# Optimization experiments

Hardware: AMD Instinct MI355X
Metric: run time of the kernel (lower is better)

The kernel has to match this reference:

```python
import jax, jax.numpy as jnp
import numpy as np

N = 400000      # total atoms across batch of molecules
E = 1600000     # directed edges (avg degree 4)
G = 4096        # number of graphs (molecules)
F_IN = 78       # atomic feature size
H = 128         # gnn hidden dims (gnn_0 = gnn_1 = 128)
FF0, FF1 = 256, 128


def _lin(k, fan_in, fan_out):
    return jax.random.normal(k, (fan_in, fan_out), jnp.float32) / np.sqrt(fan_in).astype(np.float32)


def setup_inputs() -> dict:
    key = jax.random.key(0)
    ks = jax.random.split(key, 10)
    x = jax.random.normal(ks[0], (N, F_IN), jnp.float32)
    edge_index = jax.random.randint(ks[1], (2, E), 0, N, dtype=jnp.int64)
    # sorted graph ids, guaranteed non-empty segments (empty segment -> -inf under max pool)
    batch = (jnp.arange(N, dtype=jnp.int64) * G) // N
    return {
        'x': x, 'edge_index': edge_index, 'batch': batch,
        'W0': _lin(ks[2], F_IN, H), 'b0': jnp.zeros((H,), jnp.float32),
        'W1': _lin(ks[3], H, H),    'b1': jnp.zeros((H,), jnp.float32),
        'Wf0': _lin(ks[4], H, FF0), 'bf0': jnp.zeros((FF0,), jnp.float32),
        'Wf1': _lin(ks[5], FF0, FF1), 'bf1': jnp.zeros((FF1,), jnp.float32),
    }


def _gcn_conv(h, W, b, src, dst, dinv):
    # GCNConv with add_self_loops=True, symmetric normalization.
    hw = h @ W                                     # [N, out]
    norm = dinv[src] * dinv[dst]                   # [E]
    msg = hw[src] * norm[:, None]                  # gather + scale
    agg = jax.ops.segment_sum(msg, dst, num_segments=h.shape[0])
    agg = agg + hw * (dinv * dinv)[:, None]        # self-loop contribution
    return agg + b


def reference(x, edge_index, batch, W0, b0, W1, b1, Wf0, bf0, Wf1, bf1):
    src, dst = edge_index[0], edge_index[1]
    # degree of A + I computed at target nodes (PyG gcn_norm uses col)
    deg = jax.ops.segment_sum(jnp.ones((E,), x.dtype), dst, num_segments=N) + 1.0
    dinv = jax.lax.rsqrt(deg)

    h = jax.nn.relu(_gcn_conv(x, W0, b0, src, dst, dinv))
    h = jax.nn.relu(_gcn_conv(h, W1, b1, src, dst, dinv))

    g = jax.ops.segment_max(h, batch, num_segments=G)   # global max pool [G, H]

    g = jax.nn.relu(g @ Wf0 + bf0)   # dropout is identity in eval
    g = jax.nn.relu(g @ Wf1 + bf1)
    return g
```

## Files before the change

kernel.cpp:

```cpp
#include <hip/hip_runtime.h>
#include <cstdint>
#include <cstddef>

#define NATOMS 400000
#define NEDGES 1600000
#define NGRAPH 4096
#define F_INN  78
#define HDIM   128
#define FF0D   256
#define FF1D   128

#define XPAD   80

typedef __attribute__((ext_vector_type(8))) short short8;
typedef __attribute__((ext_vector_type(4))) short short4v;
typedef __attribute__((ext_vector_type(4))) float f32x4;
typedef __attribute__((ext_vector_type(2))) float f32x2;

static __device__ __forceinline__ short f2bf(float f) {
    unsigned u = __builtin_bit_cast(unsigned, f);
    unsigned r = (u + 0x7fffu + ((u >> 16) & 1u)) >> 16;
    return (short)r;
}
static __device__ __forceinline__ float bf2f(unsigned short u) {
    return __builtin_bit_cast(float, ((unsigned)u) << 16);
}

__global__ __launch_bounds__(256) void k_degi(const int* __restrict__ dst,
                                              int* __restrict__ deg,
                                              int* __restrict__ rank, int E) {
    int e = blockIdx.x * 256 + threadIdx.x;
    if (e < E) rank[e] = atomicAdd(&deg[dst[e]], 1);
}

__global__ __launch_bounds__(256) void k_scan1(int* __restrict__ data,
                                               int* __restrict__ blockSums,
                                               float* __restrict__ dinv, int n) {
    __shared__ int ts[256];
    const int base = blockIdx.x * 1024 + threadIdx.x * 4;
    int v[4];
    #pragma unroll
    for (int j = 0; j < 4; ++j) v[j] = (base + j < n) ? data[base + j] : 0;
    #pragma unroll
    for (int j = 0; j < 4; ++j)
        if (base + j < n) dinv[base + j] = rsqrtf((float)v[j] + 1.0f);
    const int tot = v[0] + v[1] + v[2] + v[3];
    ts[threadIdx.x] = tot;
    __syncthreads();
    #pragma unroll
    for (int off = 1; off < 256; off <<= 1) {
        int t = (threadIdx.x >= off) ? ts[threadIdx.x - off] : 0;
        __syncthreads();
        ts[threadIdx.x] += t;
        __syncthreads();
    }
    int run = ts[threadIdx.x] - tot;
    #pragma unroll
    for (int j = 0; j < 4; ++j) {
        if (base + j < n) data[base + j] = run;
        run += v[j];
    }
    if (threadIdx.x == 255) blockSums[blockIdx.x] = ts[255];
}

__global__ __launch_bounds__(512) void k_scan2(int* __restrict__ blockSums, int nb) {
    __shared__ int ts[512];
    int v = (threadIdx.x < nb) ? blockSums[threadIdx.x] : 0;
    ts[threadIdx.x] = v;
    __syncthreads();
    #pragma unroll
    for (int off = 1; off < 512; off <<= 1) {
        int t = (threadIdx.x >= off) ? ts[threadIdx.x - off] : 0;
        __syncthreads();
        ts[threadIdx.x] += t;
        __syncthreads();
    }
    if (threadIdx.x < nb) blockSums[threadIdx.x] = ts[threadIdx.x] - v;
}

__global__ __launch_bounds__(256) void k_scan3(int* __restrict__ data,
                                               const int* __restrict__ blockSums,
                                               int n, int total) {
    const int off = blockSums[blockIdx.x];
    const int base = blockIdx.x * 1024 + threadIdx.x * 4;
    #pragma unroll
    for (int j = 0; j < 4; ++j)
        if (base + j < n) data[base + j] += off;
    if (blockIdx.x == 0 && threadIdx.x == 0) data[n] = total;
}

__global__ __launch_bounds__(256) void k_fill(const int* __restrict__ src,
                                              const int* __restrict__ dst,
                                              const int* __restrict__ row_start,
                                              const int* __restrict__ rank,
                                              int2* __restrict__ csr_ev,
                                              const float* __restrict__ dinv, int E) {
    int e = blockIdx.x * 256 + threadIdx.x;
    if (e >= E) return;
    int d = dst[e];
    int s = src[e];
    int pos = row_start[d] + rank[e];
    float norm = dinv[s] * dinv[d];
    csr_ev[pos] = make_int2(s, __builtin_bit_cast(int, norm));
}

template<int KC, int KSRC, bool BIASROW>
__global__ __launch_bounds__(64) void k_packw(const float* __restrict__ W,
                                              const float* __restrict__ b,
                                              short* __restrict__ wf) {
    int t = blockIdx.x * 64 + threadIdx.x;
    int f = t >> 6, lane = t & 63;
    int ct = f / KC, kc = f % KC;
    int n  = ct * 16 + (lane & 15);
    int k0 = kc * 32 + (lane >> 4) * 8;
    short8 o;
    #pragma unroll
    for (int j = 0; j < 8; ++j) {
        int k = k0 + j;
        float v = 0.f;
        if (k < KSRC) v = W[(size_t)k * 128 + n];
        else if (BIASROW && k == KSRC) v = b[n];
        o[j] = f2bf(v);
    }
    *(short8*)(wf + (size_t)t * 8) = o;
}

__global__ __launch_bounds__(256) void k_packx(const float* __restrict__ x,
                                               unsigned short* __restrict__ xb) {
    int t = blockIdx.x * 256 + threadIdx.x;
    if (t >= NATOMS * 20) return;
    int n = t / 20, g = t % 20;
    const float* xr = x + (size_t)n * F_INN + g * 4;
    short4v o;
    if (g < 19) {
        f32x2 a = *(const f32x2*)(xr);
        f32x2 b = *(const f32x2*)(xr + 2);
        o.x = f2bf(a.x); o.y = f2bf(a.y); o.z = f2bf(b.x); o.w = f2bf(b.y);
    } else {
        f32x2 a = *(const f32x2*)(xr);
        o.x = f2bf(a.x); o.y = f2bf(a.y); o.z = 0; o.w = 0;
    }
    *(short4v*)(xb + (size_t)n * XPAD + g * 4) = o;
}

__global__ __launch_bounds__(256) void k_fused0(
    const unsigned short* __restrict__ xb, const short* __restrict__ wfrag,
    const int* __restrict__ row_start, const int2* __restrict__ csr_ev,
    const float* __restrict__ dinv, short* __restrict__ outp)
{
    constexpr int XLDS = 104;
    __shared__ short lds_w[24 * 64 * 8];
    __shared__ __align__(16) unsigned short xs[32 * XLDS];
    __shared__ __align__(16) char lds_st[4 * 2048];

    const int tid = threadIdx.x;
    #pragma unroll
    for (int it = 0; it < 6; ++it) {
        int t = it * 256 + tid;
        *(short8*)(lds_w + (size_t)t * 8) = *(const short8*)(wfrag + (size_t)t * 8);
    }

    {
        const int nl = tid >> 3;
        const int n  = blockIdx.x * 32 + nl;
        const int l  = tid & 7;
        const int c8 = l * 8;
        const int ct = 64 + l * 2;
        const float dv = dinv[n];
        const float d2 = dv * dv;

        float acc[8], tacc0, tacc1;
        {
            const short8 sv = *(const short8*)(xb + (size_t)n * XPAD + c8);
            const unsigned tv = *(const unsigned*)(xb + (size_t)n * XPAD + ct);
            #pragma unroll
            for (int j = 0; j < 8; ++j) acc[j] = bf2f((unsigned short)sv[j]) * d2;
            tacc0 = bf2f((unsigned short)(tv & 0xffff)) * d2;
            tacc1 = bf2f((unsigned short)(tv >> 16)) * d2;
        }

        const int s0 = row_start[n], s1 = row_start[n + 1];
        int i = s0;
        for (; i + 3 < s1; i += 4) {
            const int2 e0 = csr_ev[i];
            const int2 e1 = csr_ev[i + 1];
            const int2 e2 = csr_ev[i + 2];
            const int2 e3 = csr_ev[i + 3];
            const short8 r0 = *(const short8*)(xb + (size_t)e0.x * XPAD + c8);
            const short8 r1 = *(const short8*)(xb + (size_t)e1.x * XPAD + c8);
            const short8 r2 = *(const short8*)(xb + (size_t)e2.x * XPAD + c8);
            const short8 r3 = *(const short8*)(xb + (size_t)e3.x * XPAD + c8);
            const unsigned t0 = *(const unsigned*)(xb + (size_t)e0.x * XPAD + ct);
            const unsigned t1 = *(const unsigned*)(xb + (size_t)e1.x * XPAD + ct);
            const unsigned t2 = *(const unsigned*)(xb + (size_t)e2.x * XPAD + ct);
            const unsigned t3 = *(const unsigned*)(xb + (size_t)e3.x * XPAD + ct);
            const float w0 = __builtin_bit_cast(float, e0.y);
            const float w1 = __builtin_bit_cast(float, e1.y);
            const float w2 = __builtin_bit_cast(float, e2.y);
            const float w3 = __builtin_bit_cast(float, e3.y);
            #pragma unroll
            for (int j = 0; j < 8; ++j) acc[j] = fmaf(bf2f((unsigned short)r0[j]), w0, acc[j]);
            #pragma unroll
            for (int j = 0; j < 8; ++j) acc[j] = fmaf(bf2f((unsigned short)r1[j]), w1, acc[j]);
            #pragma unroll
            for (int j = 0; j < 8; ++j) acc[j] = fmaf(bf2f((unsigned short)r2[j]), w2, acc[j]);
            #pragma unroll
            for (int j = 0; j < 8; ++j) acc[j] = fmaf(bf2f((unsigned short)r3[j]), w3, acc[j]);
            tacc0 = fmaf(bf2f((unsigned short)(t0 & 0xffff)), w0, tacc0);
            tacc1 = fmaf(bf2f((unsigned short)(t0 >> 16)),    w0, tacc1);
            tacc0 = fmaf(bf2f((unsigned short)(t1 & 0xffff)), w1, tacc0);
            tacc1 = fmaf(bf2f((unsigned short)(t1 >> 16)),    w1, tacc1);
            tacc0 = fmaf(bf2f((unsigned short)(t2 & 0xffff)), w2, tacc0);
            tacc1 = fmaf(bf2f((unsigned short)(t2 >> 16)),    w2, tacc1);
            tacc0 = fmaf(bf2f((unsigned short)(t3 & 0xffff)), w3, tacc0);
            tacc1 = fmaf(bf2f((unsigned short)(t3 >> 16)),    w3, tacc1);
        }
        for (; i < s1; ++i) {
            const int2 e0 = csr_ev[i];
            const short8 r0 = *(const short8*)(xb + (size_t)e0.x * XPAD + c8);
            const unsigned t0 = *(const unsigned*)(xb + (size_t)e0.x * XPAD + ct);
            const float w0 = __builtin_bit_cast(float, e0.y);
            #pragma unroll
            for (int j = 0; j < 8; ++j) acc[j] = fmaf(bf2f((unsigned short)r0[j]), w0, acc[j]);
            tacc0 = fmaf(bf2f((unsigned short)(t0 & 0xffff)), w0, tacc0);
            tacc1 = fmaf(bf2f((unsigned short)(t0 >> 16)),    w0, tacc1);
        }

        short8 o;
        #pragma unroll
        for (int j = 0; j < 8; ++j) o[j] = f2bf(acc[j]);
        *(short8*)(xs + nl * XLDS + c8) = o;
        unsigned to;
        if (l == 7) to = 0x00003F80u;
        else {
            to = (unsigned)(unsigned short)f2bf(tacc0) |
                 ((unsigned)(unsigned short)f2bf(tacc1) << 16);
        }
        *(unsigned*)(xs + nl * XLDS + ct) = to;
        *(unsigned*)(xs + nl * XLDS + 80 + l * 2) = 0u;
    }
    __syncthreads();

    const int lane = tid & 63;
    const int wid  = tid >> 6;
    const int m = lane & 15, q = lane >> 4;
    const int T  = wid >> 1;
    const int c0 = (wid & 1) * 4;

    short8 afr[3];
    #pragma unroll
    for (int kc = 0; kc < 3; ++kc)
        afr[kc] = *(const short8*)(xs + (T * 16 + m) * XLDS + kc * 32 + q * 8);

    f32x4 acc[4];
    #pragma unroll
    for (int cc = 0; cc < 4; ++cc) acc[cc] = (f32x4){0.f, 0.f, 0.f, 0.f};
    #pragma unroll
    for (int kc = 0; kc < 3; ++kc)
        #pragma unroll
        for (int cc = 0; cc < 4; ++cc) {
            const short8 wv = *(const short8*)(lds_w + ((size_t)(((c0 + cc) * 3 + kc) * 64 + lane)) * 8);
            acc[cc] = __builtin_amdgcn_mfma_f32_16x16x32_bf16(wv, afr[kc], acc[cc], 0, 0, 0);
        }

    char* const st = lds_st + wid * 2048;
    #pragma unroll
    for (int cc = 0; cc < 4; ++cc) {
        short4v o;
        o.x = f2bf(fmaxf(acc[cc][0], 0.f));
        o.y = f2bf(fmaxf(acc[cc][1], 0.f));
        o.z = f2bf(fmaxf(acc[cc][2], 0.f));
        o.w = f2bf(fmaxf(acc[cc][3], 0.f));
        const int c = (cc * 32 + q * 8) ^ ((m & 7) << 4);
        *(short4v*)(st + m * 128 + c) = o;
    }
    #pragma unroll
    for (int p = 0; p < 2; ++p) {
        const int r  = p * 8 + (lane >> 3);
        const int cb = ((lane & 7) * 16) ^ ((r & 7) << 4);
        const short8 v = *(const short8*)(st + r * 128 + cb);
        *(short8*)(outp + (size_t)(blockIdx.x * 32 + T * 16 + r) * 128
                        + c0 * 16 + (lane & 7) * 8) = v;
    }
}

template<int KC, int KSRC, bool RELU>
__global__ __launch_bounds__(256) void k_gemm_mfma(
    const short* __restrict__ inv, const short* __restrict__ wfrag,
    short* __restrict__ outp, int M)
{
    constexpr int NFRAG = 8 * KC;
    __shared__ short lds_w[NFRAG * 64 * 8];
    __shared__ __align__(16) char lds_st[4 * 4096];

    const int tid = threadIdx.x;
    #pragma unroll
    for (int it = 0; it < NFRAG * 64 / 256; ++it) {
        int t = it * 256 + tid;
        *(short8*)(lds_w + (size_t)t * 8) = *(const short8*)(wfrag + (size_t)t * 8);
    }
    __syncthreads();

    const int lane = tid & 63;
    const int m = lane & 15, q = lane >> 4;
    const int wid = tid >> 6;
    const int gw = blockIdx.x * 4 + wid;
    const int NW = gridDim.x * 4;
    const int NTILE = M / 16;
    char* const st = lds_st + wid * 4096;

    auto tile_mma = [&](int t, const short8* afr) {
        f32x4 acc[8];
        #pragma unroll
        for (int ct = 0; ct < 8; ++ct) acc[ct] = (f32x4){0.f, 0.f, 0.f, 0.f};
        #pragma unroll
        for (int kc = 0; kc < KC; ++kc)
            #pragma unroll
            for (int ct = 0; ct < 8; ++ct) {
                const short8 wv = *(const short8*)(lds_w + ((size_t)((ct * KC + kc) * 64 + lane)) * 8);
                acc[ct] = __builtin_amdgcn_mfma_f32_16x16x32_bf16(wv, afr[kc], acc[ct], 0, 0, 0);
            }
        #pragma unroll
        for (int ct = 0; ct < 8; ++ct) {
            short4v o;
            float v0 = acc[ct][0], v1 = acc[ct][1], v2 = acc[ct][2], v3 = acc[ct][3];
            if constexpr (RELU) {
                v0 = fmaxf(v0, 0.f); v1 = fmaxf(v1, 0.f);
                v2 = fmaxf(v2, 0.f); v3 = fmaxf(v3, 0.f);
            }
            o.x = f2bf(v0); o.y = f2bf(v1); o.z = f2bf(v2); o.w = f2bf(v3);
            const int c = (ct * 32 + q * 8) ^ ((m & 7) << 4);
            *(short4v*)(st + m * 256 + c) = o;
        }
        #pragma unroll
        for (int p = 0; p < 4; ++p) {
            const int r = p * 4 + (lane >> 4);
            const int c = ((lane & 15) * 16) ^ ((r & 7) << 4);
            const short8 v = *(const short8*)(st + r * 256 + c);
            *(short8*)(outp + (size_t)(t * 16 + r) * 128 + (lane & 15) * 8) = v;
        }
    };

    short8 fA[KC], fB[KC];
    auto load_to = [&](int tile, short8* b) {
        const short* xr = inv + (size_t)(tile * 16 + m) * KSRC;
        #pragma unroll
        for (int kc = 0; kc < KC; ++kc) {
            const int k0 = kc * 32 + q * 8;
            short8 v = {0, 0, 0, 0, 0, 0, 0, 0};
            if (k0 + 8 <= KSRC) v = *(const short8*)(xr + k0);
            b[kc] = v;
        }
    };

    load_to(gw, fA);
    for (int t = gw; t < NTILE; t += NW) {
        const int tn = t + NW;
        if (tn < NTILE) load_to(tn, fB);
        tile_mma(t, fA);
        #pragma unroll
        for (int kc = 0; kc < KC; ++kc) fA[kc] = fB[kc];
    }
}

__global__ __launch_bounds__(256) void k_gather_pool(
    const unsigned short* __restrict__ hw,
    const int* __restrict__ row_start, const int2* __restrict__ csr_ev,
    const float* __restrict__ dinv, const float* __restrict__ bias,
    const int* __restrict__ batch, int* __restrict__ pool, int half)
{
    const int n  = blockIdx.x * 32 + (threadIdx.x >> 3);
    const int c8 = half * 64 + (threadIdx.x & 7) * 8;
    const float dv = dinv[n];
    const float d2 = dv * dv;

    float acc[8];
    {
        const short8 sv = *(const short8*)(hw + (size_t)n * HDIM + c8);
        #pragma unroll
        for (int j = 0; j < 8; ++j)
            acc[j] = fmaf(bf2f((unsigned short)sv[j]), d2, bias[c8 + j]);
    }

    const int s0 = row_start[n], s1 = row_start[n + 1];
    int i = s0;
    for (; i + 3 < s1; i += 4) {
        const int2 e0 = csr_ev[i];
        const int2 e1 = csr_ev[i + 1];
        const int2 e2 = csr_ev[i + 2];
        const int2 e3 = csr_ev[i + 3];
        const short8 r0 = *(const short8*)(hw + (size_t)e0.x * HDIM + c8);
        const short8 r1 = *(const short8*)(hw + (size_t)e1.x * HDIM + c8);
        const short8 r2 = *(const short8*)(hw + (size_t)e2.x * HDIM + c8);
        const short8 r3 = *(const short8*)(hw + (size_t)e3.x * HDIM + c8);
        const float w0 = __builtin_bit_cast(float, e0.y);
        const float w1 = __builtin_bit_cast(float, e1.y);
        const float w2 = __builtin_bit_cast(float, e2.y);
        const float w3 = __builtin_bit_cast(float, e3.y);
        #pragma unroll
        for (int j = 0; j < 8; ++j) acc[j] = fmaf(bf2f((unsigned short)r0[j]), w0, acc[j]);
        #pragma unroll
        for (int j = 0; j < 8; ++j) acc[j] = fmaf(bf2f((unsigned short)r1[j]), w1, acc[j]);
        #pragma unroll
        for (int j = 0; j < 8; ++j) acc[j] = fmaf(bf2f((unsigned short)r2[j]), w2, acc[j]);
        #pragma unroll
        for (int j = 0; j < 8; ++j) acc[j] = fmaf(bf2f((unsigned short)r3[j]), w3, acc[j]);
    }
    for (; i < s1; ++i) {
        const int2 e0 = csr_ev[i];
        const short8 r0 = *(const short8*)(hw + (size_t)e0.x * HDIM + c8);
        const float w0 = __builtin_bit_cast(float, e0.y);
        #pragma unroll
        for (int j = 0; j < 8; ++j) acc[j] = fmaf(bf2f((unsigned short)r0[j]), w0, acc[j]);
    }

    const int gbase = batch[blockIdx.x * 32];
    const int glast = batch[blockIdx.x * 32 + 31];
    const int idx   = batch[n] - gbase;

    float red[2][8];
    #pragma unroll
    for (int s = 0; s < 2; ++s)
        #pragma unroll
        for (int j = 0; j < 8; ++j)
            red[s][j] = (idx == s) ? fmaxf(acc[j], 0.f) : 0.f;

    #pragma unroll
    for (int msk = 8; msk <= 32; msk <<= 1)
        #pragma unroll
        for (int s = 0; s < 2; ++s)
            #pragma unroll
            for (int j = 0; j < 8; ++j)
                red[s][j] = fmaxf(red[s][j], __shfl_xor(red[s][j], msk));

    __shared__ float sm[4][2][64];
    const int wid  = threadIdx.x >> 6;
    const int lane = threadIdx.x & 63;
    if (lane < 8) {
        #pragma unroll
        for (int s = 0; s < 2; ++s)
            #pragma unroll
            for (int j = 0; j < 8; ++j)
                sm[wid][s][lane * 8 + j] = red[s][j];
    }
    __syncthreads();
    if (threadIdx.x < 128) {
        const int s = threadIdx.x >> 6;
        const int f = threadIdx.x & 63;
        if (s == 0 || glast != gbase) {
            float m = fmaxf(fmaxf(sm[0][s][f], sm[1][s][f]),
                            fmaxf(sm[2][s][f], sm[3][s][f]));
            atomicMax(pool + (size_t)(gbase + s) * HDIM + half * 64 + f,
                      __builtin_bit_cast(int, m));
        }
    }
}

template<int K, int NC, bool OUT_RELU_BIAS>
__global__ __launch_bounds__(256) void k_gemm(
    const float* __restrict__ in, const float* __restrict__ W,
    const float* __restrict__ out_bias, float* __restrict__ out0, int M)
{
    constexpr int BK = 32;
    constexpr int TC = NC / 8;
    constexpr int TR = 256 / TC;
    constexpr int ROWS = TR * 8;
    constexpr int XST = ROWS + 4;

    __shared__ float xs[BK][XST];
    __shared__ float ws[BK][NC];

    const int tid = threadIdx.x;
    const int tc  = tid % TC;
    const int tr  = tid / TC;
    const int row0 = blockIdx.x * ROWS;

    float acc[8][8];
    #pragma unroll
    for (int i = 0; i < 8; ++i)
        #pragma unroll
        for (int j = 0; j < 8; ++j) acc[i][j] = 0.f;

    for (int k0 = 0; k0 < K; k0 += BK) {
        {
            constexpr int TASKS = BK * NC / 4;
            #pragma unroll
            for (int it = 0; it < TASKS / 256; ++it) {
                int t  = it * 256 + tid;
                int wk = t / (NC / 4);
                int wc = (t % (NC / 4)) * 4;
                *(float4*)(&ws[wk][wc]) = *(const float4*)(W + (size_t)(k0 + wk) * NC + wc);
            }
        }
        {
            constexpr int TASKS = ROWS * BK / 4;
            #pragma unroll
            for (int it = 0; it < TASKS / 256; ++it) {
                int t   = it * 256 + tid;
                int r   = t / (BK / 4);
                int kq  = (t % (BK / 4)) * 4;
                float4 x4 = *(const float4*)(in + (size_t)(row0 + r) * K + k0 + kq);
                xs[kq + 0][r] = x4.x; xs[kq + 1][r] = x4.y;
                xs[kq + 2][r] = x4.z; xs[kq + 3][r] = x4.w;
            }
        }
        __syncthreads();
        #pragma unroll 8
        for (int kk = 0; kk < BK; ++kk) {
            float a[8], b[8];
            #pragma unroll
            for (int i = 0; i < 8; ++i) a[i] = xs[kk][tr * 8 + i];
            #pragma unroll
            for (int j = 0; j < 8; ++j) b[j] = ws[kk][tc * 8 + j];
            #pragma unroll
            for (int i = 0; i < 8; ++i)
                #pragma unroll
                for (int j = 0; j < 8; ++j)
                    acc[i][j] = fmaf(a[i], b[j], acc[i][j]);
        }
        __syncthreads();
    }

    #pragma unroll
    for (int i = 0; i < 8; ++i) {
        const int row = row0 + tr * 8 + i;
        #pragma unroll
        for (int jq = 0; jq < 2; ++jq) {
            const int col = tc * 8 + jq * 4;
            float4 v;
            v.x = acc[i][jq * 4 + 0]; v.y = acc[i][jq * 4 + 1];
            v.z = acc[i][jq * 4 + 2]; v.w = acc[i][jq * 4 + 3];
            if constexpr (OUT_RELU_BIAS) {
                const float4 bb = *(const float4*)(out_bias + col);
                v.x = fmaxf(v.x + bb.x, 0.f); v.y = fmaxf(v.y + bb.y, 0.f);
                v.z = fmaxf(v.z + bb.z, 0.f); v.w = fmaxf(v.w + bb.w, 0.f);
            }
            *(float4*)(out0 + (size_t)row * NC + col) = v;
        }
    }
}

extern "C" void kernel_launch(void* const* d_in, const int* in_sizes, int n_in,
                              void* d_out, int out_size, void* d_ws, size_t ws_size,
                              hipStream_t stream) {
    const float* x    = (const float*)d_in[0];
    const int*   ei   = (const int*)d_in[1];
    const int*   batch= (const int*)d_in[2];
    const float* W0   = (const float*)d_in[3];
    const float* b0   = (const float*)d_in[4];
    const float* W1   = (const float*)d_in[5];
    const float* b1   = (const float*)d_in[6];
    const float* Wf0  = (const float*)d_in[7];
    const float* bf0  = (const float*)d_in[8];
    const float* Wf1  = (const float*)d_in[9];
    const float* bf1  = (const float*)d_in[10];
    float* out = (float*)d_out;

    const int* srcI = ei;
    const int* dstI = ei + NEDGES;

    constexpr int SCAN_NBLK = (NATOMS + 1023) / 1024;

    char* base = (char*)d_ws;
    unsigned short* hwA  = (unsigned short*)(base + 0);
    int*   rank      = (int*)(base + 0);
    unsigned short* aggB = (unsigned short*)(base + 102400000);
    float* dinv      = (float*)(base + 204800000);
    int*   row_start = (int*)(base + 206400000);
    int2*  csr_ev    = (int2*)(base + 208000064);
    int*   blockSums = (int*)(base + 220800064);
    float* pool      = (float*)(base + 220802112);
    float* ff0       = (float*)(base + 222899264);
    short* wf0       = (short*)(base + 227093568);
    short* wf1       = (short*)(base + 227118144);
    unsigned short* xb = (unsigned short*)(base + 227150912);

    hipMemsetAsync(row_start, 0, (size_t)(NATOMS + 1) * sizeof(int), stream);
    hipMemsetAsync(pool, 0, (size_t)NGRAPH * HDIM * sizeof(float), stream);
    k_degi<<<(NEDGES + 255) / 256, 256, 0, stream>>>(dstI, row_start, rank, NEDGES);
    k_scan1<<<SCAN_NBLK, 256, 0, stream>>>(row_start, blockSums, dinv, NATOMS);
    k_scan2<<<1, 512, 0, stream>>>(blockSums, SCAN_NBLK);
    k_scan3<<<SCAN_NBLK, 256, 0, stream>>>(row_start, blockSums, NATOMS, NEDGES);
    k_fill<<<(NEDGES + 255) / 256, 256, 0, stream>>>(srcI, dstI, row_start, rank,
                                                     csr_ev, dinv, NEDGES);

    k_packw<3, F_INN, true><<<8 * 3, 64, 0, stream>>>(W0, b0, wf0);
    k_packw<4, HDIM, false><<<8 * 4, 64, 0, stream>>>(W1, nullptr, wf1);
    k_packx<<<(NATOMS * 20 + 255) / 256, 256, 0, stream>>>(x, xb);

    k_fused0<<<NATOMS / 32, 256, 0, stream>>>(xb, wf0, row_start, csr_ev, dinv,
                                              (short*)aggB);

    k_gemm_mfma<4, HDIM, false><<<1024, 256, 0, stream>>>((const short*)aggB, wf1,
                                                          (short*)hwA, NATOMS);
    k_gather_pool<<<NATOMS / 32, 256, 0, stream>>>(hwA, row_start, csr_ev,
                                                   dinv, b1, batch, (int*)pool, 0);
    k_gather_pool<<<NATOMS / 32, 256, 0, stream>>>(hwA, row_start, csr_ev,
                                                   dinv, b1, batch, (int*)pool, 1);

    k_gemm<HDIM, FF0D, true><<<NGRAPH / 64, 256, 0, stream>>>(pool, Wf0, bf0, ff0, NGRAPH);
    k_gemm<FF0D, FF1D, true><<<NGRAPH / 128, 256, 0, stream>>>(ff0, Wf1, bf1, out, NGRAPH);
}
```

Measured before the change: 658.1 us.

## Fuse layer-2 aggregation, W1 GEMM and max-pool into one kernel

```diff
diff --git a/kernel.cpp b/kernel.cpp
--- a/kernel.cpp
+++ b/kernel.cpp
@@ -149,7 +149,7 @@
     const float* __restrict__ dinv, short* __restrict__ outp)
 {
     constexpr int XLDS = 104;
-    __shared__ short lds_w[24 * 64 * 8];
+    __shared__ __align__(16) short lds_w[24 * 64 * 8];
     __shared__ __align__(16) unsigned short xs[32 * XLDS];
     __shared__ __align__(16) char lds_st[4 * 2048];
 
@@ -284,174 +284,155 @@
     }
 }
 
-template<int KC, int KSRC, bool RELU>
-__global__ __launch_bounds__(256) void k_gemm_mfma(
-    const short* __restrict__ inv, const short* __restrict__ wfrag,
-    short* __restrict__ outp, int M)
-{
-    constexpr int NFRAG = 8 * KC;
-    __shared__ short lds_w[NFRAG * 64 * 8];
-    __shared__ __align__(16) char lds_st[4 * 4096];
-
-    const int tid = threadIdx.x;
-    #pragma unroll
-    for (int it = 0; it < NFRAG * 64 / 256; ++it) {
-        int t = it * 256 + tid;
-        *(short8*)(lds_w + (size_t)t * 8) = *(const short8*)(wfrag + (size_t)t * 8);
-    }
-    __syncthreads();
-
-    const int lane = tid & 63;
-    const int m = lane & 15, q = lane >> 4;
-    const int wid = tid >> 6;
-    const int gw = blockIdx.x * 4 + wid;
-    const int NW = gridDim.x * 4;
-    const int NTILE = M / 16;
-    char* const st = lds_st + wid * 4096;
-
-    auto tile_mma = [&](int t, const short8* afr) {
-        f32x4 acc[8];
-        #pragma unroll
-        for (int ct = 0; ct < 8; ++ct) acc[ct] = (f32x4){0.f, 0.f, 0.f, 0.f};
-        #pragma unroll
-        for (int kc = 0; kc < KC; ++kc)
-            #pragma unroll
-            for (int ct = 0; ct < 8; ++ct) {
-                const short8 wv = *(const short8*)(lds_w + ((size_t)((ct * KC + kc) * 64 + lane)) * 8);
-                acc[ct] = __builtin_amdgcn_mfma_f32_16x16x32_bf16(wv, afr[kc], acc[ct], 0, 0, 0);
-            }
-        #pragma unroll
-        for (int ct = 0; ct < 8; ++ct) {
-            short4v o;
-            float v0 = acc[ct][0], v1 = acc[ct][1], v2 = acc[ct][2], v3 = acc[ct][3];
-            if constexpr (RELU) {
-                v0 = fmaxf(v0, 0.f); v1 = fmaxf(v1, 0.f);
-                v2 = fmaxf(v2, 0.f); v3 = fmaxf(v3, 0.f);
-            }
-            o.x = f2bf(v0); o.y = f2bf(v1); o.z = f2bf(v2); o.w = f2bf(v3);
-            const int c = (ct * 32 + q * 8) ^ ((m & 7) << 4);
-            *(short4v*)(st + m * 256 + c) = o;
-        }
-        #pragma unroll
-        for (int p = 0; p < 4; ++p) {
-            const int r = p * 4 + (lane >> 4);
-            const int c = ((lane & 15) * 16) ^ ((r & 7) << 4);
-            const short8 v = *(const short8*)(st + r * 256 + c);
-            *(short8*)(outp + (size_t)(t * 16 + r) * 128 + (lane & 15) * 8) = v;
-        }
-    };
-
-    short8 fA[KC], fB[KC];
-    auto load_to = [&](int tile, short8* b) {
-        const short* xr = inv + (size_t)(tile * 16 + m) * KSRC;
-        #pragma unroll
-        for (int kc = 0; kc < KC; ++kc) {
-            const int k0 = kc * 32 + q * 8;
-            short8 v = {0, 0, 0, 0, 0, 0, 0, 0};
-            if (k0 + 8 <= KSRC) v = *(const short8*)(xr + k0);
-            b[kc] = v;
-        }
-    };
-
-    load_to(gw, fA);
-    for (int t = gw; t < NTILE; t += NW) {
-        const int tn = t + NW;
-        if (tn < NTILE) load_to(tn, fB);
-        tile_mma(t, fA);
-        #pragma unroll
-        for (int kc = 0; kc < KC; ++kc) fA[kc] = fB[kc];
-    }
-}
-
-__global__ __launch_bounds__(256) void k_gather_pool(
-    const unsigned short* __restrict__ hw,
+__global__ __launch_bounds__(512) void k_fused1(
+    const unsigned short* __restrict__ hw, const short* __restrict__ wfrag,
     const int* __restrict__ row_start, const int2* __restrict__ csr_ev,
     const float* __restrict__ dinv, const float* __restrict__ bias,
-    const int* __restrict__ batch, int* __restrict__ pool, int half)
+    const int* __restrict__ batch, int* __restrict__ pool)
 {
-    const int n  = blockIdx.x * 32 + (threadIdx.x >> 3);
-    const int c8 = half * 64 + (threadIdx.x & 7) * 8;
-    const float dv = dinv[n];
-    const float d2 = dv * dv;
-
-    float acc[8];
+    constexpr int XL = 136;
+    __shared__ __align__(16) short lds_w[32 * 64 * 8];
+    __shared__ __align__(16) unsigned short xs[64 * XL];
+
+    const int tid = threadIdx.x;
+    #pragma unroll
+    for (int it = 0; it < 4; ++it) {
+        int t = it * 512 + tid;
+        *(short8*)(lds_w + (size_t)t * 8) = *(const short8*)(wfrag + (size_t)t * 8);
+    }
+
     {
-        const short8 sv = *(const short8*)(hw + (size_t)n * HDIM + c8);
-        #pragma unroll
-        for (int j = 0; j < 8; ++j)
-            acc[j] = fmaf(bf2f((unsigned short)sv[j]), d2, bias[c8 + j]);
-    }
-
-    const int s0 = row_start[n], s1 = row_start[n + 1];
-    int i = s0;
-    for (; i + 3 < s1; i += 4) {
-        const int2 e0 = csr_ev[i];
-        const int2 e1 = csr_ev[i + 1];
-        const int2 e2 = csr_ev[i + 2];
-        const int2 e3 = csr_ev[i + 3];
-        const short8 r0 = *(const short8*)(hw + (size_t)e0.x * HDIM + c8);
-        const short8 r1 = *(const short8*)(hw + (size_t)e1.x * HDIM + c8);
-        const short8 r2 = *(const short8*)(hw + (size_t)e2.x * HDIM + c8);
-        const short8 r3 = *(const short8*)(hw + (size_t)e3.x * HDIM + c8);
-        const float w0 = __builtin_bit_cast(float, e0.y);
-        const float w1 = __builtin_bit_cast(float, e1.y);
-        const float w2 = __builtin_bit_cast(float, e2.y);
-        const float w3 = __builtin_bit_cast(float, e3.y);
-        #pragma unroll
-        for (int j = 0; j < 8; ++j) acc[j] = fmaf(bf2f((unsigned short)r0[j]), w0, acc[j]);
-        #pragma unroll
-        for (int j = 0; j < 8; ++j) acc[j] = fmaf(bf2f((unsigned short)r1[j]), w1, acc[j]);
-        #pragma unroll
-        for (int j = 0; j < 8; ++j) acc[j] = fmaf(bf2f((unsigned short)r2[j]), w2, acc[j]);
-        #pragma unroll
-        for (int j = 0; j < 8; ++j) acc[j] = fmaf(bf2f((unsigned short)r3[j]), w3, acc[j]);
-    }
-    for (; i < s1; ++i) {
-        const int2 e0 = csr_ev[i];
-        const short8 r0 = *(const short8*)(hw + (size_t)e0.x * HDIM + c8);
-        const float w0 = __builtin_bit_cast(float, e0.y);
-        #pragma unroll
-        for (int j = 0; j < 8; ++j) acc[j] = fmaf(bf2f((unsigned short)r0[j]), w0, acc[j]);
-    }
-
-    const int gbase = batch[blockIdx.x * 32];
-    const int glast = batch[blockIdx.x * 32 + 31];
-    const int idx   = batch[n] - gbase;
-
-    float red[2][8];
-    #pragma unroll
-    for (int s = 0; s < 2; ++s)
-        #pragma unroll
-        for (int j = 0; j < 8; ++j)
-            red[s][j] = (idx == s) ? fmaxf(acc[j], 0.f) : 0.f;
-
-    #pragma unroll
-    for (int msk = 8; msk <= 32; msk <<= 1)
-        #pragma unroll
-        for (int s = 0; s < 2; ++s)
-            #pragma unroll
-            for (int j = 0; j < 8; ++j)
-                red[s][j] = fmaxf(red[s][j], __shfl_xor(red[s][j], msk));
-
-    __shared__ float sm[4][2][64];
-    const int wid  = threadIdx.x >> 6;
-    const int lane = threadIdx.x & 63;
-    if (lane < 8) {
-        #pragma unroll
-        for (int s = 0; s < 2; ++s)
-            #pragma unroll
-            for (int j = 0; j < 8; ++j)
-                sm[wid][s][lane * 8 + j] = red[s][j];
+        const int nl = tid >> 3;
+        const int n  = blockIdx.x * 64 + nl;
+        const int l  = tid & 7;
+        const int cA = l * 8;
+        const int cB = 64 + l * 8;
+        const float dv = dinv[n];
+        const float d2 = dv * dv;
+
+        float aA[8], aB[8];
+        {
+            const short8 sa = *(const short8*)(hw + (size_t)n * HDIM + cA);
+            const short8 sb = *(const short8*)(hw + (size_t)n * HDIM + cB);
+            #pragma unroll
+            for (int j = 0; j < 8; ++j) {
+                aA[j] = bf2f((unsigned short)sa[j]) * d2;
+                aB[j] = bf2f((unsigned short)sb[j]) * d2;
+            }
+        }
+
+        const int s0 = row_start[n], s1 = row_start[n + 1];
+        int i = s0;
+        for (; i + 1 < s1; i += 2) {
+            const int2 e0 = csr_ev[i];
+            const int2 e1 = csr_ev[i + 1];
+            const short8 rA0 = *(const short8*)(hw + (size_t)e0.x * HDIM + cA);
+            const short8 rB0 = *(const short8*)(hw + (size_t)e0.x * HDIM + cB);
+            const short8 rA1 = *(const short8*)(hw + (size_t)e1.x * HDIM + cA);
+            const short8 rB1 = *(const short8*)(hw + (size_t)e1.x * HDIM + cB);
+            const float w0 = __builtin_bit_cast(float, e0.y);
+            const float w1 = __builtin_bit_cast(float, e1.y);
+            #pragma unroll
+            for (int j = 0; j < 8; ++j) {
+                aA[j] = fmaf(bf2f((unsigned short)rA0[j]), w0, aA[j]);
+                aB[j] = fmaf(bf2f((unsigned short)rB0[j]), w0, aB[j]);
+            }
+            #pragma unroll
+            for (int j = 0; j < 8; ++j) {
+                aA[j] = fmaf(bf2f((unsigned short)rA1[j]), w1, aA[j]);
+                aB[j] = fmaf(bf2f((unsigned short)rB1[j]), w1, aB[j]);
+            }
+        }
+        for (; i < s1; ++i) {
+            const int2 e0 = csr_ev[i];
+            const short8 rA0 = *(const short8*)(hw + (size_t)e0.x * HDIM + cA);
+            const short8 rB0 = *(const short8*)(hw + (size_t)e0.x * HDIM + cB);
+            const float w0 = __builtin_bit_cast(float, e0.y);
+            #pragma unroll
+            for (int j = 0; j < 8; ++j) {
+                aA[j] = fmaf(bf2f((unsigned short)rA0[j]), w0, aA[j]);
+                aB[j] = fmaf(bf2f((unsigned short)rB0[j]), w0, aB[j]);
+            }
+        }
+
+        short8 oA, oB;
+        #pragma unroll
+        for (int j = 0; j < 8; ++j) { oA[j] = f2bf(aA[j]); oB[j] = f2bf(aB[j]); }
+        *(short8*)(xs + nl * XL + cA) = oA;
+        *(short8*)(xs + nl * XL + cB) = oB;
     }
     __syncthreads();
-    if (threadIdx.x < 128) {
-        const int s = threadIdx.x >> 6;
-        const int f = threadIdx.x & 63;
-        if (s == 0 || glast != gbase) {
-            float m = fmaxf(fmaxf(sm[0][s][f], sm[1][s][f]),
-                            fmaxf(sm[2][s][f], sm[3][s][f]));
-            atomicMax(pool + (size_t)(gbase + s) * HDIM + half * 64 + f,
-                      __builtin_bit_cast(int, m));
+
+    const int lane = tid & 63;
+    const int wid  = tid >> 6;
+    const int m = lane & 15, q = lane >> 4;
+    const int T  = wid >> 1;
+    const int c0 = (wid & 1) * 4;
+
+    short8 afr[4];
+    #pragma unroll
+    for (int kc = 0; kc < 4; ++kc)
+        afr[kc] = *(const short8*)(xs + (T * 16 + m) * XL + kc * 32 + q * 8);
+
+    f32x4 acc[4];
+    #pragma unroll
+    for (int cc = 0; cc < 4; ++cc) acc[cc] = (f32x4){0.f, 0.f, 0.f, 0.f};
+    #pragma unroll
+    for (int kc = 0; kc < 4; ++kc)
+        #pragma unroll
+        for (int cc = 0; cc < 4; ++cc) {
+            const short8 wv = *(const short8*)(lds_w + ((size_t)(((c0 + cc) * 4 + kc) * 64 + lane)) * 8);
+            acc[cc] = __builtin_amdgcn_mfma_f32_16x16x32_bf16(wv, afr[kc], acc[cc], 0, 0, 0);
+        }
+
+    const int nb    = blockIdx.x * 64;
+    const int gbase = batch[nb];
+    const int glast = batch[nb + 63];
+    const int idx   = batch[nb + T * 16 + m] - gbase;
+
+    float v[16];
+    #pragma unroll
+    for (int cc = 0; cc < 4; ++cc) {
+        const f32x4 b4 = *(const f32x4*)(bias + (c0 + cc) * 16 + q * 4);
+        #pragma unroll
+        for (int j = 0; j < 4; ++j)
+            v[cc * 4 + j] = fmaxf(acc[cc][j] + b4[j], 0.f);
+    }
+
+    {
+        float r[16];
+        #pragma unroll
+        for (int k = 0; k < 16; ++k) r[k] = (idx == 0) ? v[k] : 0.f;
+        #pragma unroll
+        for (int msk = 1; msk <= 8; msk <<= 1)
+            #pragma unroll
+            for (int k = 0; k < 16; ++k)
+                r[k] = fmaxf(r[k], __shfl_xor(r[k], msk));
+        if (m == 0) {
+            #pragma unroll
+            for (int cc = 0; cc < 4; ++cc)
+                #pragma unroll
+                for (int j = 0; j < 4; ++j)
+                    atomicMax(pool + (size_t)gbase * HDIM + (c0 + cc) * 16 + q * 4 + j,
+                              __builtin_bit_cast(int, r[cc * 4 + j]));
+        }
+    }
+    if (glast != gbase) {
+        float r[16];
+        #pragma unroll
+        for (int k = 0; k < 16; ++k) r[k] = (idx == 1) ? v[k] : 0.f;
+        #pragma unroll
+        for (int msk = 1; msk <= 8; msk <<= 1)
+            #pragma unroll
+            for (int k = 0; k < 16; ++k)
+                r[k] = fmaxf(r[k], __shfl_xor(r[k], msk));
+        if (m == 0) {
+            #pragma unroll
+            for (int cc = 0; cc < 4; ++cc)
+                #pragma unroll
+                for (int j = 0; j < 4; ++j)
+                    atomicMax(pool + (size_t)(gbase + 1) * HDIM + (c0 + cc) * 16 + q * 4 + j,
+                              __builtin_bit_cast(int, r[cc * 4 + j]));
         }
     }
 }
@@ -562,7 +543,6 @@
     constexpr int SCAN_NBLK = (NATOMS + 1023) / 1024;
 
     char* base = (char*)d_ws;
-    unsigned short* hwA  = (unsigned short*)(base + 0);
     int*   rank      = (int*)(base + 0);
     unsigned short* aggB = (unsigned short*)(base + 102400000);
     float* dinv      = (float*)(base + 204800000);
@@ -591,12 +571,8 @@
     k_fused0<<<NATOMS / 32, 256, 0, stream>>>(xb, wf0, row_start, csr_ev, dinv,
                                               (short*)aggB);
 
-    k_gemm_mfma<4, HDIM, false><<<1024, 256, 0, stream>>>((const short*)aggB, wf1,
-                                                          (short*)hwA, NATOMS);
-    k_gather_pool<<<NATOMS / 32, 256, 0, stream>>>(hwA, row_start, csr_ev,
-                                                   dinv, b1, batch, (int*)pool, 0);
-    k_gather_pool<<<NATOMS / 32, 256, 0, stream>>>(hwA, row_start, csr_ev,
-                                                   dinv, b1, batch, (int*)pool, 1);
+    k_fused1<<<NATOMS / 64, 512, 0, stream>>>(aggB, wf1, row_start, csr_ev,
+                                              dinv, b1, batch, (int*)pool);
 
     k_gemm<HDIM, FF0D, true><<<NGRAPH / 64, 256, 0, stream>>>(pool, Wf0, bf0, ff0, NGRAPH);
     k_gemm<FF0D, FF1D, true><<<NGRAPH / 128, 256, 0, stream>>>(ff0, Wf1, bf1, out, NGRAPH);
```

Result: faster. 641.1 us (-2.6%).
